# Performance work log

Measured on AMD Instinct MI355X. Metric: run time of the kernel, lower is better.

## Reference

```python
import jax, jax.numpy as jnp
import numpy as np

HEADS = 8
GROUPS = 8            # offset_groups (defaults to heads)
DIM = 256
DIM_HEAD = 64
INNER = HEADS * DIM_HEAD          # 512
OFF_DIMS = INNER // GROUPS        # 64
DS = 4                            # downsample_factor
OFF_SCALE = float(DS)             # offset_scale defaults to downsample_factor
KS = 6                            # offset_kernel_size
SCALE = DIM_HEAD ** -0.5


def grouped_conv1x1(x, w, groups):
    # x: (B, Cin, N), w: (Cout, Cin//groups, 1) -> (B, Cout, N)
    B, Cin, N = x.shape
    Cout = w.shape[0]
    xg = x.reshape(B, groups, Cin // groups, N)
    wg = w[:, :, 0].reshape(groups, Cout // groups, Cin // groups)
    return jnp.einsum('bgin,goi->bgon', xg, wg).reshape(B, Cout, N)


def group(t, groups):
    # 'b (g d) n -> (b g) d n'
    B, C, N = t.shape
    return t.reshape(B, groups, C // groups, N).reshape(B * groups, C // groups, N)


def bilinear_sample_1d(feats, grid):
    # F.grid_sample 1d equivalent: bilinear, padding_mode='zeros', align_corners=False
    # feats: (B, C, N); grid: (B, M) in [-1, 1] -> (B, C, M)
    B, C, N = feats.shape
    pos = ((grid + 1.0) * N - 1.0) * 0.5     # unnormalized coordinate
    i0f = jnp.floor(pos)
    w1 = (pos - i0f)[:, None, :]
    i0 = i0f.astype(jnp.int32)

    def gather(idx):
        valid = ((idx >= 0) & (idx < N))[:, None, :].astype(feats.dtype)
        g = jnp.take_along_axis(feats, jnp.clip(idx, 0, N - 1)[:, None, :], axis=2)
        return g * valid

    return gather(i0) * (1.0 - w1) + gather(i0 + 1) * w1


def setup_inputs() -> dict:
    key = jax.random.key(0)
    ks = jax.random.split(key, 10)
    B, N = 4, 4096
    s = lambda k, shape, fan: jax.random.normal(k, shape, jnp.float32) * (fan ** -0.5)
    return {
        'x': jax.random.normal(ks[0], (B, N, DIM), jnp.float32),
        'prev_x': jax.random.normal(ks[1], (B, N, DIM), jnp.float32),
        'wq': s(ks[2], (INNER, 2 * DIM // GROUPS, 1), 2 * DIM // GROUPS),
        'wk': s(ks[3], (INNER, DIM // GROUPS, 1), DIM // GROUPS),
        'wv': s(ks[4], (INNER, DIM // GROUPS, 1), DIM // GROUPS),
        'wo': s(ks[5], (DIM, INNER, 1), INNER),
        'bo': jnp.zeros((DIM,), jnp.float32),
        'w_off1': s(ks[6], (OFF_DIMS, 1, KS), KS),      # depthwise conv, groups=OFF_DIMS
        'b_off1': jnp.zeros((OFF_DIMS,), jnp.float32),
        'w_off2': s(ks[7], (1, OFF_DIMS, 1), OFF_DIMS),  # 1x1 conv, no bias
    }


def reference(x, prev_x, wq, wk, wv, wo, bo, w_off1, b_off1, w_off2):
    B, N, _ = x.shape
    xt = jnp.swapaxes(x, 1, 2)        # (B, D, N)
    pt = jnp.swapaxes(prev_x, 1, 2)   # (B, D, N)
    cat = jnp.concatenate([pt, xt], axis=1)       # (B, 2D, N)

    q = grouped_conv1x1(cat, wq, GROUPS)          # (B, INNER, N)
    gq = group(q, GROUPS)                         # (B*G, OFF_DIMS, N)

    # to_offsets: depthwise conv (stride DS) -> GELU -> 1x1 -> tanh -> *scale
    pad = (KS - DS) // 2
    h = jax.lax.conv_general_dilated(
        gq, w_off1, (DS,), [(pad, pad)],
        dimension_numbers=('NCH', 'OIH', 'NCH'),
        feature_group_count=OFF_DIMS)
    h = jax.nn.gelu(h + b_off1[None, :, None], approximate=False)  # (B*G, OFF_DIMS, M)
    offsets = jnp.einsum('bcn,oc->bon', h, w_off2[:, :, 0])[:, 0]  # (B*G, M)
    offsets = jnp.tanh(offsets) * OFF_SCALE

    M = offsets.shape[-1]                          # downsampled kv length
    vgrid = jnp.arange(M, dtype=offsets.dtype) + offsets
    vgrid_scaled = 2.0 * vgrid / max(M - 1, 1) - 1.0

    kv = bilinear_sample_1d(group(pt, GROUPS), vgrid_scaled)       # (B*G, D/G, M)
    kv = kv.reshape(B, GROUPS, DIM // GROUPS, M).reshape(B, DIM, M)

    k = grouped_conv1x1(kv, wk, GROUPS)            # (B, INNER, M)
    v = grouped_conv1x1(kv, wv, GROUPS)            # (B, INNER, M)

    # 'b (h d) n -> b h n d'
    qh = (q * SCALE).reshape(B, HEADS, DIM_HEAD, N).transpose(0, 1, 3, 2)
    kh = k.reshape(B, HEADS, DIM_HEAD, M).transpose(0, 1, 3, 2)
    vh = v.reshape(B, HEADS, DIM_HEAD, M).transpose(0, 1, 3, 2)

    attn = jax.nn.softmax(jnp.einsum('bhid,bhjd->bhij', qh, kh), axis=-1)
    out = jnp.einsum('bhij,bhjd->bhid', attn, vh)  # (B, H, N, Dh)

    out = out.transpose(0, 1, 3, 2).reshape(B, INNER, N)
    out = jnp.einsum('bcn,oc->bon', out, wo[:, :, 0]) + bo[None, :, None]
    return jnp.swapaxes(out, 1, 2)                 # (B, N, D)
```

## Files before the change

kernel.cpp:

```cpp
#include <hip/hip_runtime.h>
#include <hip/hip_bf16.h>

#define NN 4096
#define DIMC 256
#define NH 8
#define MM 1024
#define SCALE 0.18033688011112042f

typedef __hip_bfloat16 bf16;
typedef __bf16 bf16x8 __attribute__((ext_vector_type(8)));
typedef __bf16 bf16x4 __attribute__((ext_vector_type(4)));
typedef float f32x4 __attribute__((ext_vector_type(4)));
#define MFMA16(a, b, c) __builtin_amdgcn_mfma_f32_16x16x32_bf16(a, b, c, 0, 0, 0)

typedef __bf16 lds_row72[72];

__device__ __forceinline__ float bf2f(bf16 v) { return __bfloat162float(v); }
__device__ __forceinline__ float ldin(const void* p, size_t i, int f) {
    return f ? __bfloat162float(((const bf16*)p)[i]) : ((const float*)p)[i];
}
__device__ __forceinline__ bf16x8 ld8bf(const void* p, size_t i, int f) {
    if (f) return *(const bf16x8*)((const __bf16*)p + i);
    const float* s = (const float*)p + i;
    float4 a = *(const float4*)s, b = *(const float4*)(s + 4);
    bf16x8 r = {(__bf16)a.x, (__bf16)a.y, (__bf16)a.z, (__bf16)a.w,
                (__bf16)b.x, (__bf16)b.y, (__bf16)b.z, (__bf16)b.w};
    return r;
}

__global__ __launch_bounds__(256) void detect_kernel(const unsigned short* __restrict__ xu,
                                                     int* __restrict__ flag) {
    __shared__ int smax;
    int t = threadIdx.x;
    if (t == 0) smax = 0;
    __syncthreads();
    int mymax = 0;
    for (int i = t; i < 4096; i += 256) {
        int e = (xu[i] >> 7) & 0xFF;
        mymax = max(mymax, e);
    }
    atomicMax(&smax, mymax);
    __syncthreads();
    if (t == 0) *flag = (smax >= 0x90) ? 0 : 1;
}

__global__ __launch_bounds__(256) void off_kernel(
    const void* __restrict__ xp, const void* __restrict__ pxp,
    const void* __restrict__ wqp, const void* __restrict__ w1p,
    const void* __restrict__ b1p, const void* __restrict__ w2p,
    float* __restrict__ offs, const int* __restrict__ flagp) {
    __shared__ __align__(16) float wq_lds[64][68];
    __shared__ __align__(16) float cat_lds[66][68];
    __shared__ float q_lds[66][68];
    int f = *flagp;
    int t = threadIdx.x;
    int bg = blockIdx.x >> 6;
    int m0 = (blockIdx.x & 63) << 4;
    int b = bg >> 3, g = bg & 7;
    const void* src = (g < 4) ? pxp : xp;
    int base = (g & 3) << 6;
    for (int idx = t; idx < 4096; idx += 256)
        wq_lds[idx >> 6][idx & 63] = ldin(wqp, g * 4096 + idx, f);
    for (int idx = t; idx < 66 * 64; idx += 256) {
        int r = idx >> 6, c = idx & 63;
        int n = 4 * m0 - 1 + r;
        cat_lds[r][c] = (n >= 0 && n < NN)
            ? ldin(src, ((size_t)b * NN + n) * DIMC + base + c, f) : 0.0f;
    }
    __syncthreads();
    {
        int tc = t & 15, tr = t >> 4;
        float acc[4][4];
#pragma unroll
        for (int a = 0; a < 4; ++a)
#pragma unroll
            for (int bb = 0; bb < 4; ++bb) acc[a][bb] = 0.f;
#pragma unroll
        for (int i4 = 0; i4 < 16; ++i4) {
            float4 cv[4], wv[4];
#pragma unroll
            for (int a = 0; a < 4; ++a)
                cv[a] = *(const float4*)&cat_lds[tr + 16 * a][i4 * 4];
#pragma unroll
            for (int bb = 0; bb < 4; ++bb)
                wv[bb] = *(const float4*)&wq_lds[tc + 16 * bb][i4 * 4];
#pragma unroll
            for (int a = 0; a < 4; ++a)
#pragma unroll
                for (int bb = 0; bb < 4; ++bb) {
                    acc[a][bb] += cv[a].x * wv[bb].x;
                    acc[a][bb] += cv[a].y * wv[bb].y;
                    acc[a][bb] += cv[a].z * wv[bb].z;
                    acc[a][bb] += cv[a].w * wv[bb].w;
                }
        }
#pragma unroll
        for (int a = 0; a < 4; ++a)
#pragma unroll
            for (int bb = 0; bb < 4; ++bb)
                q_lds[tr + 16 * a][tc + 16 * bb] = acc[a][bb];
        if (t < 128) {
            int r = 64 + (t >> 6), c = t & 63;
            float a2 = 0.f;
#pragma unroll
            for (int i4 = 0; i4 < 16; ++i4) {
                float4 cv = *(const float4*)&cat_lds[r][i4 * 4];
                float4 wv = *(const float4*)&wq_lds[c][i4 * 4];
                a2 += cv.x * wv.x;
                a2 += cv.y * wv.y;
                a2 += cv.z * wv.z;
                a2 += cv.w * wv.w;
            }
            q_lds[r][c] = a2;
        }
    }
    __syncthreads();
    int w = t >> 6, lane = t & 63;
    float w1v[6];
#pragma unroll
    for (int tap = 0; tap < 6; ++tap) w1v[tap] = ldin(w1p, lane * 6 + tap, f);
    float b1v = ldin(b1p, lane, f);
    float w2v = ldin(w2p, lane, f);
    for (int jj = 0; jj < 4; ++jj) {
        int dm = w * 4 + jj;
        int r0 = 4 * dm;
        float acc = b1v;
#pragma unroll
        for (int tap = 0; tap < 6; ++tap) acc += q_lds[r0 + tap][lane] * w1v[tap];
        float gl = 0.5f * acc * (1.0f + erff(acc * 0.70710678118654752f));
        float s = gl * w2v;
#pragma unroll
        for (int o = 32; o; o >>= 1) s += __shfl_xor(s, o);
        if (lane == 0) offs[bg * MM + m0 + dm] = tanhf(s) * 4.0f;
    }
}

__global__ __launch_bounds__(256) void kvproj_kernel(
    const void* __restrict__ pxp, const void* __restrict__ wkp,
    const void* __restrict__ wvp, const float* __restrict__ offs,
    __bf16* __restrict__ khi_g, __bf16* __restrict__ klo_g,
    __bf16* __restrict__ vt_g, const int* __restrict__ flagp) {
    __shared__ float wk_lds[64][33];
    __shared__ float wv_lds[64][33];
    __shared__ float kv_lds[64][33];
    __shared__ __align__(16) __bf16 vt_lds[64][72];
    __shared__ float offl[64];
    int f = *flagp;
    int t = threadIdx.x;
    int bh = blockIdx.x >> 4;
    int m0 = (blockIdx.x & 15) << 6;
    int b = bh >> 3, h = bh & 7;
    if (t < 64) offl[t] = offs[bh * MM + m0 + t];
    for (int kk = t; kk < 2048; kk += 256) {
        wk_lds[kk >> 5][kk & 31] = ldin(wkp, h * 2048 + kk, f);
        wv_lds[kk >> 5][kk & 31] = ldin(wvp, h * 2048 + kk, f);
    }
    __syncthreads();
    for (int idx = t; idx < 2048; idx += 256) {
        int ml = idx >> 5, i = idx & 31;
        int m = m0 + ml;
        float off = offl[ml];
        float vgrid = (float)m + off;
        float gridn = 2.0f * vgrid / 1023.0f - 1.0f;
        float pos = ((gridn + 1.0f) * 4096.0f - 1.0f) * 0.5f;
        float i0f = floorf(pos);
        float w1 = pos - i0f;
        int i0 = (int)i0f;
        size_t basep = (size_t)b * NN * DIMC + h * 32 + i;
        float v0 = (i0 >= 0 && i0 < NN) ? ldin(pxp, basep + (size_t)i0 * DIMC, f) : 0.0f;
        int i1 = i0 + 1;
        float v1 = (i1 >= 0 && i1 < NN) ? ldin(pxp, basep + (size_t)i1 * DIMC, f) : 0.0f;
        kv_lds[ml][i] = v0 * (1.0f - w1) + v1 * w1;
    }
    __syncthreads();
    int d = t & 63, msub = t >> 6;
    for (int mc = 0; mc < 16; ++mc) {
        int ml = mc * 4 + msub;
        float ak = 0.f, av = 0.f;
#pragma unroll
        for (int i = 0; i < 32; ++i) {
            float x = kv_lds[ml][i];
            ak += x * wk_lds[d][i];
            av += x * wv_lds[d][i];
        }
        int m = m0 + ml;
        __bf16 kh = (__bf16)ak;
        khi_g[(size_t)(bh * MM + m) * 64 + d] = kh;
        klo_g[(size_t)(bh * MM + m) * 64 + d] = (__bf16)(ak - (float)kh);
        vt_lds[d][ml] = (__bf16)av;
    }
    __syncthreads();
    for (int idx = t; idx < 512; idx += 256) {
        int r = idx >> 3, c8 = (idx & 7) * 8;
        *(bf16x8*)&vt_g[((size_t)bh * 64 + r) * MM + m0 + c8] =
            *(const bf16x8*)&vt_lds[r][c8];
    }
}

__global__ __launch_bounds__(256) void attn_kernel(
    const void* __restrict__ xp, const void* __restrict__ pxp,
    const void* __restrict__ wqp, const __bf16* __restrict__ khi_g,
    const __bf16* __restrict__ klo_g, const __bf16* __restrict__ vt_g,
    __bf16* __restrict__ ofb, const int* __restrict__ flagp) {
    __shared__ __align__(16) char smem[46080];
    int f = *flagp;
    int bh = blockIdx.x >> 5;
    int n0 = (blockIdx.x & 31) << 7;
    int b = bh >> 3, h = bh & 7;
    int t = threadIdx.x;
    int w = t >> 6, lane = t & 63;
    int quad = lane >> 4, l15 = lane & 15;

    lds_row72* x_lds  = (lds_row72*)smem;
    lds_row72* wq_lds = (lds_row72*)(smem + 18432);
    const void* src = (h < 4) ? pxp : xp;
    int cbase = (h & 3) << 6;
#pragma unroll
    for (int j = 0; j < 4; ++j) {
        int idx = t + j * 256;
        int r = idx >> 3, c8 = (idx & 7) * 8;
        *(bf16x8*)&x_lds[r][c8] =
            ld8bf(src, ((size_t)b * NN + n0 + r) * DIMC + cbase + c8, f);
    }
#pragma unroll
    for (int j = 0; j < 2; ++j) {
        int idx = t + j * 256;
        int r = idx >> 3, c8 = (idx & 7) * 8;
        *(bf16x8*)&wq_lds[r][c8] = ld8bf(wqp, h * 4096 + r * 64 + c8, f);
    }
    __syncthreads();
    bf16x8 axf[2][2], bwf[4][2];
#pragma unroll
    for (int ms = 0; ms < 2; ++ms)
#pragma unroll
        for (int ks = 0; ks < 2; ++ks)
            axf[ms][ks] = *(const bf16x8*)&x_lds[w * 32 + ms * 16 + l15][quad * 8 + ks * 32];
#pragma unroll
    for (int ns = 0; ns < 4; ++ns)
#pragma unroll
        for (int ks = 0; ks < 2; ++ks)
            bwf[ns][ks] = *(const bf16x8*)&wq_lds[ns * 16 + l15][quad * 8 + ks * 32];
    __syncthreads();
    lds_row72* qhi = (lds_row72*)smem;
    lds_row72* qlo = (lds_row72*)(smem + 18432);
#pragma unroll
    for (int ms = 0; ms < 2; ++ms)
#pragma unroll
        for (int ns = 0; ns < 4; ++ns) {
            f32x4 acc = {0.f, 0.f, 0.f, 0.f};
            acc = MFMA16(axf[ms][0], bwf[ns][0], acc);
            acc = MFMA16(axf[ms][1], bwf[ns][1], acc);
            int col = ns * 16 + l15;
#pragma unroll
            for (int reg = 0; reg < 4; ++reg) {
                int row = w * 32 + ms * 16 + quad * 4 + reg;
                float v = acc[reg] * SCALE;
                __bf16 hi = (__bf16)v;
                qhi[row][col] = hi;
                qlo[row][col] = (__bf16)(v - (float)hi);
            }
        }
    __syncthreads();
    bf16x8 qh[2][2], ql[2][2];
#pragma unroll
    for (int ms = 0; ms < 2; ++ms)
#pragma unroll
        for (int ks = 0; ks < 2; ++ks) {
            qh[ms][ks] = *(const bf16x8*)&qhi[w * 32 + ms * 16 + l15][quad * 8 + ks * 32];
            ql[ms][ks] = *(const bf16x8*)&qlo[w * 32 + ms * 16 + l15][quad * 8 + ks * 32];
        }

    lds_row72* khi = (lds_row72*)smem;
    lds_row72* klo = (lds_row72*)(smem + 9216);
    lds_row72* vt  = (lds_row72*)(smem + 18432);
    lds_row72* p_w = (lds_row72*)(smem + 27648 + w * 4608);

    float l_run[2][4] = {{0.f, 0.f, 0.f, 0.f}, {0.f, 0.f, 0.f, 0.f}};
    f32x4 oc[2][4];
#pragma unroll
    for (int ms = 0; ms < 2; ++ms)
#pragma unroll
        for (int nd = 0; nd < 4; ++nd) oc[ms][nd] = (f32x4){0.f, 0.f, 0.f, 0.f};

    const __bf16* khb = khi_g + (size_t)bh * MM * 64;
    const __bf16* klb = klo_g + (size_t)bh * MM * 64;
    const __bf16* vtb = vt_g + (size_t)bh * 64 * MM;

    int pr0 = t >> 3, pc0 = (t & 7) * 8;
    int pr1 = (t + 256) >> 3, pc1 = pc0;
    bf16x8 pk[2], pl[2], pv[2];
    {
        pk[0] = *(const bf16x8*)&khb[(size_t)pr0 * 64 + pc0];
        pk[1] = *(const bf16x8*)&khb[(size_t)pr1 * 64 + pc1];
        pl[0] = *(const bf16x8*)&klb[(size_t)pr0 * 64 + pc0];
        pl[1] = *(const bf16x8*)&klb[(size_t)pr1 * 64 + pc1];
        pv[0] = *(const bf16x8*)&vtb[(size_t)pr0 * MM + pc0];
        pv[1] = *(const bf16x8*)&vtb[(size_t)pr1 * MM + pc1];
    }

    for (int mt = 0; mt < 16; ++mt) {
        __syncthreads();
        *(bf16x8*)&khi[pr0][pc0] = pk[0];
        *(bf16x8*)&khi[pr1][pc1] = pk[1];
        *(bf16x8*)&klo[pr0][pc0] = pl[0];
        *(bf16x8*)&klo[pr1][pc1] = pl[1];
        *(bf16x8*)&vt[pr0][pc0]  = pv[0];
        *(bf16x8*)&vt[pr1][pc1]  = pv[1];
        __syncthreads();
        if (mt < 15) {
            int m1 = (mt + 1) * 64;
            pk[0] = *(const bf16x8*)&khb[(size_t)(m1 + pr0) * 64 + pc0];
            pk[1] = *(const bf16x8*)&khb[(size_t)(m1 + pr1) * 64 + pc1];
            pl[0] = *(const bf16x8*)&klb[(size_t)(m1 + pr0) * 64 + pc0];
            pl[1] = *(const bf16x8*)&klb[(size_t)(m1 + pr1) * 64 + pc1];
            pv[0] = *(const bf16x8*)&vtb[(size_t)pr0 * MM + m1 + pc0];
            pv[1] = *(const bf16x8*)&vtb[(size_t)pr1 * MM + m1 + pc1];
        }
        f32x4 s[2][4];
#pragma unroll
        for (int ms = 0; ms < 2; ++ms)
#pragma unroll
            for (int nk = 0; nk < 4; ++nk) s[ms][nk] = (f32x4){0.f, 0.f, 0.f, 0.f};
#pragma unroll
        for (int nk = 0; nk < 4; ++nk)
#pragma unroll
            for (int ks = 0; ks < 2; ++ks) {
                bf16x8 kh = *(const bf16x8*)&khi[nk * 16 + l15][quad * 8 + ks * 32];
                bf16x8 kl = *(const bf16x8*)&klo[nk * 16 + l15][quad * 8 + ks * 32];
#pragma unroll
                for (int ms = 0; ms < 2; ++ms) {
                    s[ms][nk] = MFMA16(qh[ms][ks], kh, s[ms][nk]);
                    s[ms][nk] = MFMA16(qh[ms][ks], kl, s[ms][nk]);
                    s[ms][nk] = MFMA16(ql[ms][ks], kh, s[ms][nk]);
                }
            }
#pragma unroll
        for (int ms = 0; ms < 2; ++ms)
#pragma unroll
            for (int reg = 0; reg < 4; ++reg) {
                float p0 = exp2f(s[ms][0][reg] - 16.f);
                float p1 = exp2f(s[ms][1][reg] - 16.f);
                float p2 = exp2f(s[ms][2][reg] - 16.f);
                float p3 = exp2f(s[ms][3][reg] - 16.f);
                float ps = p0 + p1 + p2 + p3;
                ps += __shfl_xor(ps, 1);
                ps += __shfl_xor(ps, 2);
                ps += __shfl_xor(ps, 4);
                ps += __shfl_xor(ps, 8);
                l_run[ms][reg] += ps;
                int row = ms * 16 + quad * 4 + reg;
                p_w[row][l15]      = (__bf16)p0;
                p_w[row][l15 + 16] = (__bf16)p1;
                p_w[row][l15 + 32] = (__bf16)p2;
                p_w[row][l15 + 48] = (__bf16)p3;
            }
        asm volatile("s_waitcnt lgkmcnt(0)" ::: "memory");
        bf16x8 pf[2][2];
#pragma unroll
        for (int ms = 0; ms < 2; ++ms)
#pragma unroll
            for (int ks = 0; ks < 2; ++ks)
                pf[ms][ks] = *(const bf16x8*)&p_w[ms * 16 + l15][quad * 8 + ks * 32];
#pragma unroll
        for (int nd = 0; nd < 4; ++nd)
#pragma unroll
            for (int ks = 0; ks < 2; ++ks) {
                bf16x8 vf_ = *(const bf16x8*)&vt[nd * 16 + l15][quad * 8 + ks * 32];
#pragma unroll
                for (int ms = 0; ms < 2; ++ms)
                    oc[ms][nd] = MFMA16(pf[ms][ks], vf_, oc[ms][nd]);
            }
    }
#pragma unroll
    for (int ms = 0; ms < 2; ++ms)
#pragma unroll
        for (int reg = 0; reg < 4; ++reg) {
            float rl = 1.0f / l_run[ms][reg];
            int n = n0 + w * 32 + ms * 16 + quad * 4 + reg;
#pragma unroll
            for (int nd = 0; nd < 4; ++nd)
                ofb[((size_t)b * NN + n) * 512 + h * 64 + nd * 16 + l15] =
                    (__bf16)(oc[ms][nd][reg] * rl);
        }
}

__global__ __launch_bounds__(256) void o_proj_kernel(
    const __bf16* __restrict__ ofb, const void* __restrict__ wop,
    const void* __restrict__ bop, void* __restrict__ out,
    const int* __restrict__ flagp) {
    __shared__ __align__(16) char smem[27648];
    lds_row72* ahi = (lds_row72*)smem;
    lds_row72* bwo = (lds_row72*)(smem + 18432);
    int f = *flagp;
    int t = threadIdx.x;
    int row0 = (blockIdx.x >> 2) * 128;
    int o0 = (blockIdx.x & 3) * 64;
    int w = t >> 6, lane = t & 63;
    int quad = lane >> 4, l15 = lane & 15;

    f32x4 oc[2][4];
#pragma unroll
    for (int ms = 0; ms < 2; ++ms)
#pragma unroll
        for (int nd = 0; nd < 4; ++nd) oc[ms][nd] = (f32x4){0.f, 0.f, 0.f, 0.f};

    for (int k0 = 0; k0 < 512; k0 += 64) {
        if (k0) __syncthreads();
#pragma unroll
        for (int j = 0; j < 4; ++j) {
            int idx = t + j * 256;
            int r = idx >> 3, c8 = (idx & 7) * 8;
            *(bf16x8*)&ahi[r][c8] =
                *(const bf16x8*)&ofb[(size_t)(row0 + r) * 512 + k0 + c8];
        }
#pragma unroll
        for (int j = 0; j < 2; ++j) {
            int idx = t + j * 256;
            int o = idx >> 3, c8 = (idx & 7) * 8;
            *(bf16x8*)&bwo[o][c8] = ld8bf(wop, (size_t)(o0 + o) * 512 + k0 + c8, f);
        }
        __syncthreads();
        bf16x8 af[2][2], bf_[4][2];
#pragma unroll
        for (int ms = 0; ms < 2; ++ms)
#pragma unroll
            for (int ks = 0; ks < 2; ++ks)
                af[ms][ks] = *(const bf16x8*)&ahi[w * 32 + ms * 16 + l15][quad * 8 + ks * 32];
#pragma unroll
        for (int nd = 0; nd < 4; ++nd)
#pragma unroll
            for (int ks = 0; ks < 2; ++ks)
                bf_[nd][ks] = *(const bf16x8*)&bwo[nd * 16 + l15][quad * 8 + ks * 32];
#pragma unroll
        for (int ms = 0; ms < 2; ++ms)
#pragma unroll
            for (int nd = 0; nd < 4; ++nd)
#pragma unroll
                for (int ks = 0; ks < 2; ++ks)
                    oc[ms][nd] = MFMA16(af[ms][ks], bf_[nd][ks], oc[ms][nd]);
    }
    float bias[4];
#pragma unroll
    for (int nd = 0; nd < 4; ++nd) bias[nd] = ldin(bop, o0 + nd * 16 + l15, f);
#pragma unroll
    for (int ms = 0; ms < 2; ++ms)
#pragma unroll
        for (int reg = 0; reg < 4; ++reg) {
            int grow = row0 + w * 32 + ms * 16 + quad * 4 + reg;
#pragma unroll
            for (int nd = 0; nd < 4; ++nd) {
                float v = oc[ms][nd][reg] + bias[nd];
                int o = o0 + nd * 16 + l15;
                if (f) ((bf16*)out)[(size_t)grow * 256 + o] = __float2bfloat16(v);
                else   ((float*)out)[(size_t)grow * 256 + o] = v;
            }
        }
}

extern "C" void kernel_launch(void* const* d_in, const int* in_sizes, int n_in,
                              void* d_out, int out_size, void* d_ws, size_t ws_size,
                              hipStream_t stream) {
    char* W = (char*)d_ws;
    int* flag = (int*)W;
    __bf16* khi_g = (__bf16*)(W + 256);
    __bf16* klo_g = khi_g + 2097152;
    __bf16* vt_g  = klo_g + 2097152;
    __bf16* ofb   = vt_g + 2097152;
    float* offs = (float*)(ofb + 8388608);

    hipLaunchKernelGGL(detect_kernel, dim3(1), dim3(256), 0, stream,
                       (const unsigned short*)d_in[0], flag);
    hipLaunchKernelGGL(off_kernel, dim3(2048), dim3(256), 0, stream,
                       d_in[0], d_in[1], d_in[2], d_in[7], d_in[8], d_in[9],
                       offs, flag);
    hipLaunchKernelGGL(kvproj_kernel, dim3(512), dim3(256), 0, stream,
                       d_in[1], d_in[3], d_in[4], offs, khi_g, klo_g, vt_g, flag);
    hipLaunchKernelGGL(attn_kernel, dim3(1024), dim3(256), 0, stream,
                       d_in[0], d_in[1], d_in[2], khi_g, klo_g, vt_g, ofb, flag);
    hipLaunchKernelGGL(o_proj_kernel, dim3(512), dim3(256), 0, stream,
                       ofb, d_in[5], d_in[6], d_out, flag);
}
```

Measured before the change: 286.3 us.

## Keep softmax probabilities in registers via transposed QK MFMA and permlane swaps

```diff
diff --git a/kernel.cpp b/kernel.cpp
--- a/kernel.cpp
+++ b/kernel.cpp
@@ -11,7 +11,12 @@
 typedef __bf16 bf16x8 __attribute__((ext_vector_type(8)));
 typedef __bf16 bf16x4 __attribute__((ext_vector_type(4)));
 typedef float f32x4 __attribute__((ext_vector_type(4)));
+typedef unsigned u32x4 __attribute__((ext_vector_type(4)));
 #define MFMA16(a, b, c) __builtin_amdgcn_mfma_f32_16x16x32_bf16(a, b, c, 0, 0, 0)
+
+#define CVTPK(d, a, b) asm("v_cvt_pk_bf16_f32 %0, %1, %2" : "=v"(d) : "v"(a), "v"(b))
+#define SWAP32(a, b) asm("v_permlane32_swap_b32 %0, %1" : "+v"(a), "+v"(b))
+#define SWAP16(a, b) asm("v_permlane16_swap_b32 %0, %1" : "+v"(a), "+v"(b))
 
 typedef __bf16 lds_row72[72];
 
@@ -197,12 +202,12 @@
     }
 }
 
-__global__ __launch_bounds__(256) void attn_kernel(
+__global__ __launch_bounds__(256, 4) void attn_kernel(
     const void* __restrict__ xp, const void* __restrict__ pxp,
     const void* __restrict__ wqp, const __bf16* __restrict__ khi_g,
     const __bf16* __restrict__ klo_g, const __bf16* __restrict__ vt_g,
     __bf16* __restrict__ ofb, const int* __restrict__ flagp) {
-    __shared__ __align__(16) char smem[46080];
+    __shared__ __align__(16) char smem[36864];
     int f = *flagp;
     int bh = blockIdx.x >> 5;
     int n0 = (blockIdx.x & 31) << 7;
@@ -273,9 +278,8 @@
     lds_row72* khi = (lds_row72*)smem;
     lds_row72* klo = (lds_row72*)(smem + 9216);
     lds_row72* vt  = (lds_row72*)(smem + 18432);
-    lds_row72* p_w = (lds_row72*)(smem + 27648 + w * 4608);
-
-    float l_run[2][4] = {{0.f, 0.f, 0.f, 0.f}, {0.f, 0.f, 0.f, 0.f}};
+
+    float l_run[2] = {0.f, 0.f};
     f32x4 oc[2][4];
 #pragma unroll
     for (int ms = 0; ms < 2; ++ms)
@@ -329,38 +333,41 @@
                 bf16x8 kl = *(const bf16x8*)&klo[nk * 16 + l15][quad * 8 + ks * 32];
 #pragma unroll
                 for (int ms = 0; ms < 2; ++ms) {
-                    s[ms][nk] = MFMA16(qh[ms][ks], kh, s[ms][nk]);
-                    s[ms][nk] = MFMA16(qh[ms][ks], kl, s[ms][nk]);
-                    s[ms][nk] = MFMA16(ql[ms][ks], kh, s[ms][nk]);
+                    s[ms][nk] = MFMA16(kh, qh[ms][ks], s[ms][nk]);
+                    s[ms][nk] = MFMA16(kl, qh[ms][ks], s[ms][nk]);
+                    s[ms][nk] = MFMA16(kh, ql[ms][ks], s[ms][nk]);
                 }
             }
-#pragma unroll
-        for (int ms = 0; ms < 2; ++ms)
-#pragma unroll
-            for (int reg = 0; reg < 4; ++reg) {
-                float p0 = exp2f(s[ms][0][reg] - 16.f);
-                float p1 = exp2f(s[ms][1][reg] - 16.f);
-                float p2 = exp2f(s[ms][2][reg] - 16.f);
-                float p3 = exp2f(s[ms][3][reg] - 16.f);
-                float ps = p0 + p1 + p2 + p3;
-                ps += __shfl_xor(ps, 1);
-                ps += __shfl_xor(ps, 2);
-                ps += __shfl_xor(ps, 4);
-                ps += __shfl_xor(ps, 8);
-                l_run[ms][reg] += ps;
-                int row = ms * 16 + quad * 4 + reg;
-                p_w[row][l15]      = (__bf16)p0;
-                p_w[row][l15 + 16] = (__bf16)p1;
-                p_w[row][l15 + 32] = (__bf16)p2;
-                p_w[row][l15 + 48] = (__bf16)p3;
-            }
-        asm volatile("s_waitcnt lgkmcnt(0)" ::: "memory");
         bf16x8 pf[2][2];
 #pragma unroll
-        for (int ms = 0; ms < 2; ++ms)
-#pragma unroll
-            for (int ks = 0; ks < 2; ++ks)
-                pf[ms][ks] = *(const bf16x8*)&p_w[ms * 16 + l15][quad * 8 + ks * 32];
+        for (int ms = 0; ms < 2; ++ms) {
+            float ps = 0.f;
+#pragma unroll
+            for (int nk = 0; nk < 4; ++nk)
+#pragma unroll
+                for (int reg = 0; reg < 4; ++reg) {
+                    float v = exp2f(s[ms][nk][reg] - 16.f);
+                    s[ms][nk][reg] = v;
+                    ps += v;
+                }
+            ps += __shfl_xor(ps, 16);
+            ps += __shfl_xor(ps, 32);
+            l_run[ms] += ps;
+#pragma unroll
+            for (int ks = 0; ks < 2; ++ks) {
+                unsigned a0, a1, b0, b1;
+                CVTPK(a0, s[ms][2 * ks][0], s[ms][2 * ks][1]);
+                CVTPK(a1, s[ms][2 * ks][2], s[ms][2 * ks][3]);
+                CVTPK(b0, s[ms][2 * ks + 1][0], s[ms][2 * ks + 1][1]);
+                CVTPK(b1, s[ms][2 * ks + 1][2], s[ms][2 * ks + 1][3]);
+                SWAP32(a0, b0);
+                SWAP32(a1, b1);
+                SWAP16(a0, b0);
+                SWAP16(a1, b1);
+                u32x4 wrd = {a0, a1, b0, b1};
+                pf[ms][ks] = *(const bf16x8*)&wrd;
+            }
+        }
 #pragma unroll
         for (int nd = 0; nd < 4; ++nd)
 #pragma unroll
@@ -375,7 +382,8 @@
     for (int ms = 0; ms < 2; ++ms)
 #pragma unroll
         for (int reg = 0; reg < 4; ++reg) {
-            float rl = 1.0f / l_run[ms][reg];
+            float lsum = __shfl(l_run[ms], quad * 4 + reg);
+            float rl = 1.0f / lsum;
             int n = n0 + w * 32 + ms * 16 + quad * 4 + reg;
 #pragma unroll
             for (int nd = 0; nd < 4; ++nd)
```

After: 265.7 us. -7.2%, faster.
